# Kernel optimization log

Hardware: AMD Instinct MI355X
Metric: run time of the kernel (lower is better)

## Reference

```python
import jax, jax.numpy as jnp
import numpy as np

N_TOKENS = 32768
DIM = 2048
N_EXPERTS = 256
N_GROUPS = 8
N_LIMITED_GROUPS = 4
TOP_K = 8
ROUTE_SCALE = 2.5


def setup_inputs() -> dict:
    key = jax.random.key(0)
    k1, k2, k3, k4 = jax.random.split(key, 4)
    x = jax.random.normal(k1, (N_TOKENS, DIM), dtype=jnp.float32)
    w1 = jax.random.normal(k2, (N_EXPERTS, DIM), dtype=jnp.float32) * (DIM ** -0.5)
    b_lin = jax.random.normal(k3, (N_EXPERTS,), dtype=jnp.float32) * 0.02
    bias = jax.random.normal(k4, (N_EXPERTS,), dtype=jnp.float32) * 0.02
    return {"x": x, "w1": w1, "b_lin": b_lin, "bias": bias}


def reference(x, w1, b_lin, bias):
    n = x.shape[0]
    # gate GEMM: [N, dim] x [dim, E] -> [N, E]
    logits = jnp.einsum("nd,ed->ne", x, w1) + b_lin
    # sigmoid scoring with L1 normalization
    s = jax.nn.sigmoid(logits)
    s = s / jnp.sum(s, axis=-1, keepdims=True)
    # routing-correction bias (torch code adds it in place, so it is also in the
    # gathered values via the original_scores alias)
    s = s + bias
    original_scores = s
    # group-limited masking: keep only top n_limited_groups groups (amax score,
    # since use_bias=True)
    g = s.reshape(n, N_GROUPS, N_EXPERTS // N_GROUPS)
    group_scores = jnp.max(g, axis=-1)                      # [N, G]
    _, gidx = jax.lax.top_k(group_scores, N_LIMITED_GROUPS)  # [N, Glim]
    keep = jnp.zeros((n, N_GROUPS), dtype=bool).at[
        jnp.arange(n)[:, None], gidx].set(True)
    masked = jnp.where(keep[:, :, None], g, -jnp.inf).reshape(n, N_EXPERTS)
    # final top-k over masked scores, gather from (bias-added) original scores
    _, indices = jax.lax.top_k(masked, TOP_K)               # [N, k]
    values = jnp.take_along_axis(original_scores, indices, axis=1) * ROUTE_SCALE
    return values.astype(x.dtype), indices
```

## Files before the change

kernel.cpp:

```cpp
#include <hip/hip_runtime.h>
#include <math.h>

#define NTOK   32768
#define DIM    2048
#define NE     256
#define NG     8
#define GSZ    32
#define NLIM   4
#define TOPK   8
#define RSCALE 2.5f
#define TAU    4e-7f

#define BT      32
#define THREADS 256
#define KT      16
#define NKT     (DIM / KT)
#define WOFF    262144
#define TILE_B  16384

typedef __bf16 bf16x8 __attribute__((ext_vector_type(8)));
typedef float  f32x16 __attribute__((ext_vector_type(16)));

__global__ __launch_bounds__(256) void wsplit_kernel(
    const float* __restrict__ w1, unsigned int* __restrict__ wt)
{
    const int g  = blockIdx.x * 256 + threadIdx.x;
    const int e  = g & 255;
    const int hi = (g >> 8) & 1;
    const int p  = (g >> 9) & 1;
    const int kt = g >> 10;
    const float* src = w1 + (size_t)e * DIM + kt * 16 + hi * 8;

    uint4 o;
    unsigned int w[4];
#pragma unroll
    for (int q = 0; q < 4; ++q) {
        const float v0 = src[2 * q], v1 = src[2 * q + 1];
        const unsigned int u0 = __float_as_uint(v0);
        const unsigned int u1 = __float_as_uint(v1);
        if (p == 0) {
            w[q] = (u0 >> 16) | (u1 & 0xFFFF0000u);
        } else {
            const float r0 = v0 - __uint_as_float(u0 & 0xFFFF0000u);
            const float r1 = v1 - __uint_as_float(u1 & 0xFFFF0000u);
            w[q] = (__float_as_uint(r0) >> 16) |
                   (__float_as_uint(r1) & 0xFFFF0000u);
        }
    }
    o.x = w[0]; o.y = w[1]; o.z = w[2]; o.w = w[3];
    *(uint4*)(wt + (size_t)g * 4) = o;
}

__global__ __launch_bounds__(THREADS, 4) void router_pass1(
    const float* __restrict__ x, const unsigned int* __restrict__ wt,
    const float* __restrict__ b_lin, const float* __restrict__ bias,
    float* __restrict__ out_vals, float* __restrict__ out_idx,
    int* __restrict__ wsI)
{
    __shared__ union {
        unsigned short xs[2][2][32][16];
        float sc[32 * 260];
    } sm;

    const int tid  = threadIdx.x;
    const int lane = tid & 63;
    const int wn   = tid >> 6;
    const int l31  = lane & 31;
    const int hi   = lane >> 5;
    const int t0   = blockIdx.x * BT;

    const int xtok = tid >> 3, xk2 = tid & 7;
    const float2* xg = (const float2*)(x + (size_t)(t0 + xtok) * DIM) + xk2;

    const char* wb = (const char*)wt + hi * 4096 + (wn * 64 + l31) * 16;

    auto LOADB = [&](bf16x8 B[2][2], int kt) {
#pragma unroll
        for (int ni = 0; ni < 2; ++ni)
#pragma unroll
            for (int p = 0; p < 2; ++p)
                B[ni][p] = *(const bf16x8*)(wb + (size_t)kt * TILE_B +
                                            ni * 512 + p * 8192);
    };
    auto XWRITE = [&](int b, float2 v) {
        const unsigned int u0 = __float_as_uint(v.x);
        const unsigned int u1 = __float_as_uint(v.y);
        const unsigned int hp = (u0 >> 16) | (u1 & 0xFFFF0000u);
        const float r0 = v.x - __uint_as_float(u0 & 0xFFFF0000u);
        const float r1 = v.y - __uint_as_float(u1 & 0xFFFF0000u);
        const unsigned int rp = (__float_as_uint(r0) >> 16) |
                                (__float_as_uint(r1) & 0xFFFF0000u);
        *(unsigned int*)&sm.xs[b][0][xtok][xk2 * 2] = hp;
        *(unsigned int*)&sm.xs[b][1][xtok][xk2 * 2] = rp;
    };

    f32x16 acc[2] = {};

    auto COMP = [&](bf16x8 B[2][2], int cur) {
        bf16x8 ah = *(const bf16x8*)&sm.xs[cur][0][l31][hi * 8];
        bf16x8 ar = *(const bf16x8*)&sm.xs[cur][1][l31][hi * 8];
#pragma unroll
        for (int ni = 0; ni < 2; ++ni) {
            acc[ni] = __builtin_amdgcn_mfma_f32_32x32x16_bf16(ah, B[ni][0], acc[ni], 0, 0, 0);
            acc[ni] = __builtin_amdgcn_mfma_f32_32x32x16_bf16(ah, B[ni][1], acc[ni], 0, 0, 0);
            acc[ni] = __builtin_amdgcn_mfma_f32_32x32x16_bf16(ar, B[ni][0], acc[ni], 0, 0, 0);
        }
    };
    auto BARRIER = [&]() {
        __builtin_amdgcn_sched_barrier(0);
        asm volatile("s_waitcnt lgkmcnt(0)");
        __builtin_amdgcn_sched_barrier(0);
        __builtin_amdgcn_s_barrier();
        __builtin_amdgcn_sched_barrier(0);
    };

    bf16x8 BA[2][2], BB[2][2];
    float2 xo, xe;

    LOADB(BA, 0);
    float2 xv = xg[0];
    XWRITE(0, xv);
    LOADB(BB, 1);
    xo = xg[8];
    BARRIER();

    for (int kt = 0; kt < NKT; kt += 2) {
        if (kt + 1 < NKT) XWRITE(1, xo);
        if (kt + 2 < NKT) xe = xg[(kt + 2) * 8];
        COMP(BA, 0);
        if (kt + 2 < NKT) LOADB(BA, kt + 2);
        BARRIER();
        if (kt + 2 < NKT) XWRITE(0, xe);
        if (kt + 3 < NKT) xo = xg[(kt + 3) * 8];
        COMP(BB, 1);
        if (kt + 3 < NKT) LOADB(BB, kt + 3);
        BARRIER();
    }

    __syncthreads();

    const int tx = tid & 31;
    const int ty = tid >> 5;
    float blv[8], bsv[8];
#pragma unroll
    for (int j = 0; j < 8; ++j) {
        blv[j] = b_lin[tx + 32 * j];
        bsv[j] = bias[tx + 32 * j];
    }

#pragma unroll
    for (int ni = 0; ni < 2; ++ni) {
#pragma unroll
        for (int r = 0; r < 16; ++r) {
            const int row = (r & 3) + 8 * (r >> 2) + 4 * hi;
            const int e   = wn * 64 + ni * 32 + l31;
            sm.sc[row * 260 + e] = acc[ni][r];
        }
    }
    __syncthreads();

#pragma unroll
    for (int i = 0; i < 4; ++i) {
        const int row = ty * 4 + i;
        float s8[8];
        float psum = 0.0f;
#pragma unroll
        for (int j = 0; j < 8; ++j) {
            const float lg = sm.sc[row * 260 + tx + 32 * j] + blv[j];
            const float s = 1.0f / (1.0f + expf(-lg));
            s8[j] = s;
            psum += s;
        }
#pragma unroll
        for (int m = 1; m <= 16; m <<= 1) psum += __shfl_xor(psum, m);
#pragma unroll
        for (int j = 0; j < 8; ++j) s8[j] = s8[j] / psum + bsv[j];

        float gm[8];
#pragma unroll
        for (int j = 0; j < 8; ++j) gm[j] = s8[j];
#pragma unroll
        for (int m = 1; m <= 16; m <<= 1)
#pragma unroll
            for (int j = 0; j < 8; ++j)
                gm[j] = fmaxf(gm[j], __shfl_xor(gm[j], m));

        unsigned keep = 0u;
        float g4v = 0.0f, g5v = 0.0f;
#pragma unroll
        for (int r = 0; r < 5; ++r) {
            float bv = -1e30f; int bg = 0;
#pragma unroll
            for (int g = 0; g < 8; ++g)
                if (!((keep >> g) & 1) && gm[g] > bv) { bv = gm[g]; bg = g; }
            if (r < 4) { keep |= 1u << bg; g4v = bv; }
            else g5v = bv;
        }
        float margin = g4v - g5v;

#pragma unroll
        for (int j = 0; j < 8; ++j)
            if (!((keep >> j) & 1)) s8[j] = -1e30f;

        float tv[9]; int te[9];
#pragma unroll
        for (int r = 0; r < 9; ++r) {
            float bv = -1e30f; int bj = 8;
#pragma unroll
            for (int j = 0; j < 8; ++j)
                if (s8[j] > bv) { bv = s8[j]; bj = j; }
            int be = (bj < 8) ? (tx + 32 * bj) : 9999;
#pragma unroll
            for (int m = 1; m <= 16; m <<= 1) {
                const float ov = __shfl_xor(bv, m);
                const int   oe = __shfl_xor(be, m);
                if (ov > bv || (ov == bv && oe < be)) { bv = ov; be = oe; }
            }
            tv[r] = bv; te[r] = be;
            if (r < 8 && (be & 31) == tx) s8[be >> 5] = -1e30f;
        }
#pragma unroll
        for (int r = 0; r < 8; ++r) margin = fminf(margin, tv[r] - tv[r + 1]);

        if (tx == 0) {
            const int t = t0 + row;
            const int base = t * TOPK;
#pragma unroll
            for (int r = 0; r < 8; ++r) {
                out_vals[base + r] = tv[r] * RSCALE;
                out_idx[base + r]  = (float)te[r];
            }
            if (margin < TAU) {
                const int slot = atomicAdd(&wsI[0], 1);
                if (slot < 60000) wsI[4 + slot] = t;
            }
        }
    }
}

__global__ __launch_bounds__(256, 1) void router_pass2(
    const float* __restrict__ x, const float* __restrict__ w1,
    const float* __restrict__ b_lin, const float* __restrict__ bias,
    float* __restrict__ out_vals, float* __restrict__ out_idx,
    const int* __restrict__ wsI)
{
    __shared__ double xrow[DIM];
    __shared__ double red[256];
    __shared__ double sc[NE];

    const int tid = threadIdx.x;
    const int count = min(wsI[0], 60000);
    const int* list = wsI + 4;
    const float4* x4 = (const float4*)x;
    const float4* w4 = (const float4*)w1;

    for (int li = blockIdx.x; li < count; li += gridDim.x) {
        const int t = list[li];
        __syncthreads();
#pragma unroll
        for (int q = 0; q < 2; ++q) {
            const int id = tid + 256 * q;
            const float4 v = x4[t * 512 + id];
            xrow[id * 4 + 0] = (double)v.x;
            xrow[id * 4 + 1] = (double)v.y;
            xrow[id * 4 + 2] = (double)v.z;
            xrow[id * 4 + 3] = (double)v.w;
        }
        __syncthreads();

        const int e = tid;
        double a0 = 0.0, a1 = 0.0, a2 = 0.0, a3 = 0.0;
#pragma unroll 2
        for (int k4 = 0; k4 < 512; k4 += 4) {
#pragma unroll
            for (int z = 0; z < 4; ++z) {
                const float4 wv = w4[e * 512 + k4 + z];
                double* ac = (z == 0) ? &a0 : (z == 1) ? &a1 : (z == 2) ? &a2 : &a3;
                *ac = fma(xrow[(k4 + z) * 4 + 0], (double)wv.x, *ac);
                *ac = fma(xrow[(k4 + z) * 4 + 1], (double)wv.y, *ac);
                *ac = fma(xrow[(k4 + z) * 4 + 2], (double)wv.z, *ac);
                *ac = fma(xrow[(k4 + z) * 4 + 3], (double)wv.w, *ac);
            }
        }
        const double lg = ((a0 + a1) + (a2 + a3)) + (double)b_lin[e];
        const double s = 1.0 / (1.0 + exp(-lg));
        red[tid] = s;
        __syncthreads();
        for (int off = 128; off > 0; off >>= 1) {
            if (tid < off) red[tid] += red[tid + off];
            __syncthreads();
        }
        sc[e] = s / red[0] + (double)bias[e];
        __syncthreads();

        if (tid == 0) {
            double gmax[NG];
            for (int g = 0; g < NG; ++g) {
                double mx = -INFINITY;
                for (int q = 0; q < GSZ; ++q) {
                    const double v = sc[g * GSZ + q];
                    mx = (v > mx) ? v : mx;
                }
                gmax[g] = mx;
            }
            unsigned keep = 0u;
            for (int r = 0; r < NLIM; ++r) {
                int best = 0; double bv = -INFINITY;
                for (int g = 0; g < NG; ++g) {
                    if (keep & (1u << g)) continue;
                    if (gmax[g] > bv) { bv = gmax[g]; best = g; }
                }
                keep |= 1u << best;
            }
            double tv[TOPK]; int ti[TOPK];
            for (int r = 0; r < TOPK; ++r) { tv[r] = -INFINITY; ti[r] = NE; }
            for (int g = 0; g < NG; ++g) {
                if (!(keep & (1u << g))) continue;
                for (int q = 0; q < GSZ; ++q) {
                    const int ee = g * GSZ + q;
                    const double v = sc[ee];
                    if (v > tv[TOPK - 1]) {
                        int p = TOPK - 1;
                        while (p > 0 && v > tv[p - 1]) {
                            tv[p] = tv[p - 1]; ti[p] = ti[p - 1]; --p;
                        }
                        tv[p] = v; ti[p] = ee;
                    }
                }
            }
            const int base = t * TOPK;
            for (int r = 0; r < TOPK; ++r) {
                out_vals[base + r] = (float)(tv[r] * (double)RSCALE);
                out_idx[base + r]  = (float)ti[r];
            }
        }
    }
}

extern "C" void kernel_launch(void* const* d_in, const int* in_sizes, int n_in,
                              void* d_out, int out_size, void* d_ws, size_t ws_size,
                              hipStream_t stream) {
    const float* x     = (const float*)d_in[0];
    const float* w1    = (const float*)d_in[1];
    const float* b_lin = (const float*)d_in[2];
    const float* bias  = (const float*)d_in[3];
    float* out_vals = (float*)d_out;
    float* out_idx  = (float*)d_out + (size_t)NTOK * TOPK;

    int* wsI = (int*)d_ws;
    unsigned int* wt = (unsigned int*)((char*)d_ws + WOFF);

    hipMemsetAsync(d_ws, 0, 16, stream);
    wsplit_kernel<<<dim3(512), 256, 0, stream>>>(w1, wt);
    router_pass1<<<dim3(NTOK / BT), THREADS, 0, stream>>>(
        x, wt, b_lin, bias, out_vals, out_idx, wsI);
    router_pass2<<<dim3(256), 256, 0, stream>>>(
        x, w1, b_lin, bias, out_vals, out_idx, (const int*)d_ws);
}
```

Baseline: 269.7 us.

## Load x directly into MFMA registers, dropping LDS staging and barriers

Result: slower. 324.8 us (+20.4%).

```diff
diff --git a/kernel.cpp b/kernel.cpp
--- a/kernel.cpp
+++ b/kernel.cpp
@@ -51,16 +51,30 @@
     *(uint4*)(wt + (size_t)g * 4) = o;
 }
 
+__device__ __forceinline__ void split_pack(float4 a, float4 b,
+                                           bf16x8& h8, bf16x8& r8) {
+    float v[8] = {a.x, a.y, a.z, a.w, b.x, b.y, b.z, b.w};
+    union { unsigned int u[4]; bf16x8 v8; } H, R;
+#pragma unroll
+    for (int q = 0; q < 4; ++q) {
+        const unsigned int u0 = __float_as_uint(v[2 * q]);
+        const unsigned int u1 = __float_as_uint(v[2 * q + 1]);
+        H.u[q] = (u0 >> 16) | (u1 & 0xFFFF0000u);
+        const float r0 = v[2 * q]     - __uint_as_float(u0 & 0xFFFF0000u);
+        const float r1 = v[2 * q + 1] - __uint_as_float(u1 & 0xFFFF0000u);
+        R.u[q] = (__float_as_uint(r0) >> 16) |
+                 (__float_as_uint(r1) & 0xFFFF0000u);
+    }
+    h8 = H.v8; r8 = R.v8;
+}
+
 __global__ __launch_bounds__(THREADS, 4) void router_pass1(
     const float* __restrict__ x, const unsigned int* __restrict__ wt,
     const float* __restrict__ b_lin, const float* __restrict__ bias,
     float* __restrict__ out_vals, float* __restrict__ out_idx,
     int* __restrict__ wsI)
 {
-    __shared__ union {
-        unsigned short xs[2][2][32][16];
-        float sc[32 * 260];
-    } sm;
+    __shared__ float sc[32 * 260];
 
     const int tid  = threadIdx.x;
     const int lane = tid & 63;
@@ -69,74 +83,39 @@
     const int hi   = lane >> 5;
     const int t0   = blockIdx.x * BT;
 
-    const int xtok = tid >> 3, xk2 = tid & 7;
-    const float2* xg = (const float2*)(x + (size_t)(t0 + xtok) * DIM) + xk2;
-
+    const float4* xA = (const float4*)(x + (size_t)(t0 + l31) * DIM) + hi * 2;
     const char* wb = (const char*)wt + hi * 4096 + (wn * 64 + l31) * 16;
 
-    auto LOADB = [&](bf16x8 B[2][2], int kt) {
-#pragma unroll
-        for (int ni = 0; ni < 2; ++ni)
-#pragma unroll
-            for (int p = 0; p < 2; ++p)
-                B[ni][p] = *(const bf16x8*)(wb + (size_t)kt * TILE_B +
-                                            ni * 512 + p * 8192);
-    };
-    auto XWRITE = [&](int b, float2 v) {
-        const unsigned int u0 = __float_as_uint(v.x);
-        const unsigned int u1 = __float_as_uint(v.y);
-        const unsigned int hp = (u0 >> 16) | (u1 & 0xFFFF0000u);
-        const float r0 = v.x - __uint_as_float(u0 & 0xFFFF0000u);
-        const float r1 = v.y - __uint_as_float(u1 & 0xFFFF0000u);
-        const unsigned int rp = (__float_as_uint(r0) >> 16) |
-                                (__float_as_uint(r1) & 0xFFFF0000u);
-        *(unsigned int*)&sm.xs[b][0][xtok][xk2 * 2] = hp;
-        *(unsigned int*)&sm.xs[b][1][xtok][xk2 * 2] = rp;
-    };
-
     f32x16 acc[2] = {};
 
-    auto COMP = [&](bf16x8 B[2][2], int cur) {
-        bf16x8 ah = *(const bf16x8*)&sm.xs[cur][0][l31][hi * 8];
-        bf16x8 ar = *(const bf16x8*)&sm.xs[cur][1][l31][hi * 8];
-#pragma unroll
-        for (int ni = 0; ni < 2; ++ni) {
-            acc[ni] = __builtin_amdgcn_mfma_f32_32x32x16_bf16(ah, B[ni][0], acc[ni], 0, 0, 0);
-            acc[ni] = __builtin_amdgcn_mfma_f32_32x32x16_bf16(ah, B[ni][1], acc[ni], 0, 0, 0);
-            acc[ni] = __builtin_amdgcn_mfma_f32_32x32x16_bf16(ar, B[ni][0], acc[ni], 0, 0, 0);
-        }
-    };
-    auto BARRIER = [&]() {
-        __builtin_amdgcn_sched_barrier(0);
-        asm volatile("s_waitcnt lgkmcnt(0)");
-        __builtin_amdgcn_sched_barrier(0);
-        __builtin_amdgcn_s_barrier();
-        __builtin_amdgcn_sched_barrier(0);
-    };
-
-    bf16x8 BA[2][2], BB[2][2];
-    float2 xo, xe;
-
-    LOADB(BA, 0);
-    float2 xv = xg[0];
-    XWRITE(0, xv);
-    LOADB(BB, 1);
-    xo = xg[8];
-    BARRIER();
-
-    for (int kt = 0; kt < NKT; kt += 2) {
-        if (kt + 1 < NKT) XWRITE(1, xo);
-        if (kt + 2 < NKT) xe = xg[(kt + 2) * 8];
-        COMP(BA, 0);
-        if (kt + 2 < NKT) LOADB(BA, kt + 2);
-        BARRIER();
-        if (kt + 2 < NKT) XWRITE(0, xe);
-        if (kt + 3 < NKT) xo = xg[(kt + 3) * 8];
-        COMP(BB, 1);
-        if (kt + 3 < NKT) LOADB(BB, kt + 3);
-        BARRIER();
-    }
-
+#pragma unroll 4
+    for (int kt = 0; kt < NKT; ++kt) {
+        const float4 f0 = xA[kt * 4];
+        const float4 f1 = xA[kt * 4 + 1];
+        const char* pB = wb + (size_t)kt * TILE_B;
+        const bf16x8 b0h = *(const bf16x8*)(pB);
+        const bf16x8 b0r = *(const bf16x8*)(pB + 8192);
+        const bf16x8 b1h = *(const bf16x8*)(pB + 512);
+        const bf16x8 b1r = *(const bf16x8*)(pB + 512 + 8192);
+        bf16x8 ah, ar;
+        split_pack(f0, f1, ah, ar);
+        acc[0] = __builtin_amdgcn_mfma_f32_32x32x16_bf16(ah, b0h, acc[0], 0, 0, 0);
+        acc[0] = __builtin_amdgcn_mfma_f32_32x32x16_bf16(ah, b0r, acc[0], 0, 0, 0);
+        acc[0] = __builtin_amdgcn_mfma_f32_32x32x16_bf16(ar, b0h, acc[0], 0, 0, 0);
+        acc[1] = __builtin_amdgcn_mfma_f32_32x32x16_bf16(ah, b1h, acc[1], 0, 0, 0);
+        acc[1] = __builtin_amdgcn_mfma_f32_32x32x16_bf16(ah, b1r, acc[1], 0, 0, 0);
+        acc[1] = __builtin_amdgcn_mfma_f32_32x32x16_bf16(ar, b1h, acc[1], 0, 0, 0);
+    }
+
+#pragma unroll
+    for (int ni = 0; ni < 2; ++ni) {
+#pragma unroll
+        for (int r = 0; r < 16; ++r) {
+            const int row = (r & 3) + 8 * (r >> 2) + 4 * hi;
+            const int e   = wn * 64 + ni * 32 + l31;
+            sc[row * 260 + e] = acc[ni][r];
+        }
+    }
     __syncthreads();
 
     const int tx = tid & 31;
@@ -147,17 +126,6 @@
         blv[j] = b_lin[tx + 32 * j];
         bsv[j] = bias[tx + 32 * j];
     }
-
-#pragma unroll
-    for (int ni = 0; ni < 2; ++ni) {
-#pragma unroll
-        for (int r = 0; r < 16; ++r) {
-            const int row = (r & 3) + 8 * (r >> 2) + 4 * hi;
-            const int e   = wn * 64 + ni * 32 + l31;
-            sm.sc[row * 260 + e] = acc[ni][r];
-        }
-    }
-    __syncthreads();
 
 #pragma unroll
     for (int i = 0; i < 4; ++i) {
@@ -166,7 +134,7 @@
         float psum = 0.0f;
 #pragma unroll
         for (int j = 0; j < 8; ++j) {
-            const float lg = sm.sc[row * 260 + tx + 32 * j] + blv[j];
+            const float lg = sc[row * 260 + tx + 32 * j] + blv[j];
             const float s = 1.0f / (1.0f + expf(-lg));
             s8[j] = s;
             psum += s;
```
